# Performance work log

Measured on AMD Instinct MI355X. Metric: run time of the kernel, lower is better.

The kernel has to match this reference:

```python
import jax, jax.numpy as jnp
import numpy as np


def setup_inputs() -> dict:
    key = jax.random.key(0)
    k1, k2 = jax.random.split(key)
    B, S, K, N = 2, 4096, 4096, 4096
    x = jax.random.randint(k1, (B, S, K), -127, 128, dtype=jnp.int32).astype(jnp.int8)
    weight = jax.random.randint(k2, (N, K), -127, 128, dtype=jnp.int32).astype(jnp.int8)
    bias = jnp.zeros((1, N), dtype=jnp.int8)
    a = jnp.float32(0.01)   # alpha = input_scale * weight_scale / output_scale
    b = jnp.float32(1.0)    # beta = bias_scale / output_scale
    return {"x": x, "weight": weight, "bias": bias, "a": a, "b": b}


def reference(x, weight, bias, a, b):
    # i8gemm.linear_a8_w8_b8_o8: int8 GEMM with int32 accumulation, then
    # y_int8 = saturate_cast(round(alpha * acc + beta * bias)).
    x_shape = x.shape
    xf = x.reshape(-1, x_shape[-1])                     # [M, K] int8
    acc = jnp.matmul(xf, weight.T, preferred_element_type=jnp.int32)  # [M, N]
    y = a * acc.astype(jnp.float32) + b * bias.astype(jnp.float32)    # fused epilogue
    yq = jnp.clip(jnp.round(y), -128.0, 127.0).astype(jnp.int8)       # requantize o8
    return yq.reshape(*x_shape[:-1], -1)
```

## Files before the change

kernel.cpp:

```cpp
#include <hip/hip_runtime.h>
#include <stdint.h>

#define M_DIM 8192
#define N_DIM 4096
#define K_DIM 4096

using int4v = __attribute__((ext_vector_type(4))) int;

__global__ __launch_bounds__(256) void pack_kernel(const int4* __restrict__ sx,
                                                   const int4* __restrict__ sw,
                                                   unsigned int* __restrict__ dst,
                                                   int nx, int ntot) {
    int idx = blockIdx.x * blockDim.x + threadIdx.x;
    if (idx >= ntot) return;
    int4 v = (idx < nx) ? sx[idx] : sw[idx - nx];
    dst[idx] = (v.x & 0xff) | ((v.y & 0xff) << 8) | ((v.z & 0xff) << 16) |
               ((v.w & 0xff) << 24);
}

__device__ __forceinline__ void async_copy16(const char* g, char* l) {
    __builtin_amdgcn_global_load_lds(
        (const __attribute__((address_space(1))) char*)g,
        (__attribute__((address_space(3))) char*)l, 16, 0, 0);
}

__global__ __launch_bounds__(512, 4) void gemm_i8_kernel(
    const char* __restrict__ Aq,
    const char* __restrict__ Bq,
    const int* __restrict__ bias,
    const float* __restrict__ a_ptr,
    const float* __restrict__ b_ptr,
    int32_t* __restrict__ out)
{
    __shared__ char As0[256 * 64];
    __shared__ char As1[256 * 64];
    __shared__ char Bs0[128 * 64];
    __shared__ char Bs1[128 * 64];

    const int tid  = threadIdx.x;
    const int lane = tid & 63;
    const int wave = tid >> 6;
    const int wr   = wave >> 1;
    const int wc   = wave & 1;

    const int bid = blockIdx.x;
    const int xcd = bid & 7;
    const int lin = bid >> 3;
    const int mt  = (xcd & 3) * 8 + (lin & 7);
    const int nt  = (xcd >> 2) * 16 + (lin >> 3);
    const int m0  = mt * 256;
    const int n0  = nt * 128;

    const float alpha = *a_ptr;
    const float beta  = *b_ptr;

    int4v acc[4][4] = {};

    const int fr   = lane & 15;
    const int gw   = lane >> 4;
    const int koff = ((gw ^ ((fr >> 1) & 3)) << 4);
    const int aoff = (wr * 64 + fr) * 64 + koff;
    const int boff = (wc * 64 + fr) * 64 + koff;

    const int srow = tid >> 2;
    const int scg  = ((tid & 3) ^ ((tid >> 3) & 3)) << 4;
    const char* gA0 = Aq + (size_t)(m0 + srow) * K_DIM + scg;
    const char* gA1 = gA0 + (size_t)128 * K_DIM;
    const char* gB0 = Bq + (size_t)(n0 + srow) * K_DIM + scg;

#define STAGE(AS, BS, t)                                                     \
    {                                                                        \
        const size_t off_ = (size_t)(t) * 64;                                \
        async_copy16(gA0 + off_, &AS[tid * 16]);                             \
        async_copy16(gA1 + off_, &AS[8192 + tid * 16]);                      \
        async_copy16(gB0 + off_, &BS[tid * 16]);                             \
    }

#define COMPUTE(AS, BS)                                                      \
    {                                                                        \
        int4v af[4], bf[4];                                                  \
        _Pragma("unroll") for (int i = 0; i < 4; ++i)                        \
            af[i] = *(const int4v*)&AS[aoff + i * 1024];                     \
        _Pragma("unroll") for (int j = 0; j < 4; ++j)                        \
            bf[j] = *(const int4v*)&BS[boff + j * 1024];                     \
        __builtin_amdgcn_s_setprio(1);                                       \
        _Pragma("unroll") for (int i = 0; i < 4; ++i)                        \
        _Pragma("unroll") for (int j = 0; j < 4; ++j)                        \
            acc[i][j] = __builtin_amdgcn_mfma_i32_16x16x64_i8(               \
                af[i], bf[j], acc[i][j], 0, 0, 0);                           \
        __builtin_amdgcn_s_setprio(0);                                       \
    }

#define STEP_END                                                             \
    {                                                                        \
        asm volatile("s_waitcnt vmcnt(0)" ::: "memory");                     \
        __builtin_amdgcn_s_barrier();                                        \
        __builtin_amdgcn_sched_barrier(0);                                   \
    }

    STAGE(As0, Bs0, 0);
    STEP_END;

#pragma unroll 1
    for (int it = 0; it < 31; ++it) {
        STAGE(As1, Bs1, 2 * it + 1);
        __builtin_amdgcn_sched_barrier(0);
        COMPUTE(As0, Bs0);
        STEP_END;
        STAGE(As0, Bs0, 2 * it + 2);
        __builtin_amdgcn_sched_barrier(0);
        COMPUTE(As1, Bs1);
        STEP_END;
    }
    STAGE(As1, Bs1, 63);
    __builtin_amdgcn_sched_barrier(0);
    COMPUTE(As0, Bs0);
    STEP_END;
    COMPUTE(As1, Bs1);

    const int orow = (lane >> 4) * 4;
    const int ocol = lane & 15;
#pragma unroll
    for (int j = 0; j < 4; ++j) {
        const int gn = n0 + wc * 64 + j * 16 + ocol;
        const float bb = beta * (float)bias[gn];
#pragma unroll
        for (int i = 0; i < 4; ++i) {
            const int gm = m0 + wr * 64 + i * 16 + orow;
#pragma unroll
            for (int r = 0; r < 4; ++r) {
                float v = alpha * (float)acc[i][j][r] + bb;
                v = rintf(v);
                v = fminf(fmaxf(v, -128.0f), 127.0f);
                out[(size_t)(gm + r) * N_DIM + gn] = (int32_t)v;
            }
        }
    }
}

extern "C" void kernel_launch(void* const* d_in, const int* in_sizes, int n_in,
                              void* d_out, int out_size, void* d_ws, size_t ws_size,
                              hipStream_t stream) {
    const int*   x    = (const int*)d_in[0];
    const int*   w    = (const int*)d_in[1];
    const int*   bias = (const int*)d_in[2];
    const float* a    = (const float*)d_in[3];
    const float* b    = (const float*)d_in[4];
    int32_t*     out  = (int32_t*)d_out;

    char* xq = (char*)d_ws;
    const int nx   = (M_DIM * K_DIM) / 4;
    const int nw   = (N_DIM * K_DIM) / 4;
    const int ntot = nx + nw;
    pack_kernel<<<(ntot + 255) / 256, 256, 0, stream>>>(
        (const int4*)x, (const int4*)w, (unsigned int*)xq, nx, ntot);

    char* wq = xq + (size_t)M_DIM * K_DIM;

    dim3 grid((M_DIM / 256) * (N_DIM / 128));
    gemm_i8_kernel<<<grid, 512, 0, stream>>>(xq, wq, bias, a, b, out);
}
```

Measured before the change: 408.1 us.

## Deepen LDS pipeline to triple buffering with partial vmcnt waits

Adds a third LDS buffer pair so global-to-LDS loads for tile t+2 are in flight while tile t is computed. Each step now waits only until the oldest batch of async copies has landed (vmcnt(3)) instead of draining all outstanding loads. This is meant to hide more global memory latency. In exchange, LDS use per block rises from 48 KB to 72 KB, which may cut the number of resident blocks per CU and so reduce occupancy.

```diff
diff --git a/kernel.cpp b/kernel.cpp
--- a/kernel.cpp
+++ b/kernel.cpp
@@ -34,8 +34,10 @@
 {
     __shared__ char As0[256 * 64];
     __shared__ char As1[256 * 64];
+    __shared__ char As2[256 * 64];
     __shared__ char Bs0[128 * 64];
     __shared__ char Bs1[128 * 64];
+    __shared__ char Bs2[128 * 64];
 
     const int tid  = threadIdx.x;
     const int lane = tid & 63;
@@ -74,6 +76,7 @@
         async_copy16(gA0 + off_, &AS[tid * 16]);                             \
         async_copy16(gA1 + off_, &AS[8192 + tid * 16]);                      \
         async_copy16(gB0 + off_, &BS[tid * 16]);                             \
+        __builtin_amdgcn_sched_barrier(0);                                   \
     }
 
 #define COMPUTE(AS, BS)                                                      \
@@ -91,7 +94,14 @@
         __builtin_amdgcn_s_setprio(0);                                       \
     }
 
-#define STEP_END                                                             \
+#define STEP_END_CNT                                                         \
+    {                                                                        \
+        asm volatile("s_waitcnt vmcnt(3)" ::: "memory");                     \
+        __builtin_amdgcn_s_barrier();                                        \
+        __builtin_amdgcn_sched_barrier(0);                                   \
+    }
+
+#define STEP_END_ALL                                                         \
     {                                                                        \
         asm volatile("s_waitcnt vmcnt(0)" ::: "memory");                     \
         __builtin_amdgcn_s_barrier();                                        \
@@ -99,24 +109,33 @@
     }
 
     STAGE(As0, Bs0, 0);
-    STEP_END;
+    STAGE(As1, Bs1, 1);
+    asm volatile("s_waitcnt vmcnt(3)" ::: "memory");
+    __builtin_amdgcn_s_barrier();
+    __builtin_amdgcn_sched_barrier(0);
 
 #pragma unroll 1
-    for (int it = 0; it < 31; ++it) {
-        STAGE(As1, Bs1, 2 * it + 1);
-        __builtin_amdgcn_sched_barrier(0);
+    for (int i = 0; i < 20; ++i) {
+        const int t = 3 * i;
+        STAGE(As2, Bs2, t + 2);
         COMPUTE(As0, Bs0);
-        STEP_END;
-        STAGE(As0, Bs0, 2 * it + 2);
-        __builtin_amdgcn_sched_barrier(0);
+        STEP_END_CNT;
+        STAGE(As0, Bs0, t + 3);
         COMPUTE(As1, Bs1);
-        STEP_END;
+        STEP_END_CNT;
+        STAGE(As1, Bs1, t + 4);
+        COMPUTE(As2, Bs2);
+        STEP_END_CNT;
     }
-    STAGE(As1, Bs1, 63);
-    __builtin_amdgcn_sched_barrier(0);
+    STAGE(As2, Bs2, 62);
     COMPUTE(As0, Bs0);
-    STEP_END;
+    STEP_END_CNT;
+    STAGE(As0, Bs0, 63);
     COMPUTE(As1, Bs1);
+    STEP_END_CNT;
+    COMPUTE(As2, Bs2);
+    STEP_END_ALL;
+    COMPUTE(As0, Bs0);
 
     const int orow = (lane >> 4) * 4;
     const int ocol = lane & 15;
```

Result: no change. 403.5 us (-1.1%).
